# Kernel tuning notes

Measured on AMD Instinct MI355X. Metric: run time of the kernel, lower is better.

The kernel has to match this reference:

```python
import jax, jax.numpy as jnp
import numpy as np

N = 8192   # nodes per graph batch
D = 128    # node_feat_dim
E = 131072 # edges per graph batch
B = 64     # graphs per batch


def _linear_init(k, fin, fout):
    s = 1.0 / np.sqrt(fin)
    kw, kb = jax.random.split(k)
    W = jax.random.uniform(kw, (fin, fout), jnp.float32, -s, s)
    b = jax.random.uniform(kb, (fout,), jnp.float32, -s, s)
    return W, b


def setup_inputs() -> dict:
    key = jax.random.key(0)
    ks = jax.random.split(key, 10)
    x1 = jax.random.normal(ks[0], (N, D), jnp.float32)
    x2 = jax.random.normal(ks[1], (N, D), jnp.float32)
    edge_index1 = jax.random.randint(ks[2], (2, E), 0, N)
    edge_index2 = jax.random.randint(ks[3], (2, E), 0, N)
    # block-contiguous graph ids; every graph id present on both sides
    batch = jnp.arange(N, dtype=jnp.int32) // (N // B)
    mW1, mb1 = _linear_init(ks[4], 2 * D, 512)
    mW2, mb2 = _linear_init(ks[5], 512, 256)  # 256 == 2*D (update_net constraint)
    uW1, ub1 = _linear_init(ks[6], 4 * D, 512)
    uW2, ub2 = _linear_init(ks[7], 512, 256)
    uW3, ub3 = _linear_init(ks[8], 256, D)
    return dict(x1=x1, edge_index1=edge_index1, batch1=batch,
                x2=x2, edge_index2=edge_index2, batch2=batch,
                mW1=mW1, mb1=mb1, mW2=mW2, mb2=mb2,
                uW1=uW1, ub1=ub1, uW2=uW2, ub2=ub2, uW3=uW3, ub3=ub3)


def _message_aggr(x, edge_index, mW1, mb1, mW2, mb2):
    tgt, src = edge_index[0], edge_index[1]
    inp = jnp.concatenate([x[src], x[tgt]], axis=-1)          # [E, 2D]
    msg = jax.nn.relu(inp @ mW1 + mb1) @ mW2 + mb2            # [E, 2D]
    return jax.ops.segment_sum(msg, tgt, num_segments=x.shape[0])


def _cross_attention(x1, batch1, x2, batch2):
    scores = x1 @ x2.T                                        # [N1, N2]
    mask = batch1[:, None] == batch2[None, :]
    scores = jnp.where(mask, scores, -jnp.inf)
    att1 = x1 - jax.nn.softmax(scores, axis=1) @ x2
    att2 = x2 - jax.nn.softmax(scores, axis=0).T @ x1
    return att1, att2


def _node_update(x, messages, attentions, uW1, ub1, uW2, ub2, uW3, ub3):
    u = jnp.concatenate([messages, attentions, x], axis=-1)   # [N, 4D]
    h = jax.nn.relu(u @ uW1 + ub1)
    h = jax.nn.relu(h @ uW2 + ub2)
    return x + h @ uW3 + ub3                                  # residual update


def reference(x1, edge_index1, batch1, x2, edge_index2, batch2,
              mW1, mb1, mW2, mb2, uW1, ub1, uW2, ub2, uW3, ub3):
    m1 = _message_aggr(x1, edge_index1, mW1, mb1, mW2, mb2)
    m2 = _message_aggr(x2, edge_index2, mW1, mb1, mW2, mb2)
    a1, a2 = _cross_attention(x1, batch1, x2, batch2)
    new_x1 = _node_update(x1, m1, a1, uW1, ub1, uW2, ub2, uW3, ub3)
    new_x2 = _node_update(x2, m2, a2, uW1, ub1, uW2, ub2, uW3, ub3)
    return new_x1, new_x2
```

## Files before the change

### kernel.cpp

```cpp
#include <hip/hip_runtime.h>
#include <stdint.h>


typedef unsigned short u16;
typedef __bf16 bf16x8 __attribute__((ext_vector_type(8)));
typedef float f32x4 __attribute__((ext_vector_type(4)));

#define NN 8192
#define DD 128
#define EE 131072
#define GS 128
#define NG 64

__device__ __forceinline__ float bf2f(u16 u){
  return __uint_as_float(((uint32_t)u) << 16);
}
__device__ __forceinline__ u16 f2bf(float f){
  uint32_t x = __float_as_uint(f);
  return (u16)((x + 0x7fffu + ((x >> 16) & 1u)) >> 16);
}
__device__ __forceinline__ void gload16(const u16* g, u16* l){
  __builtin_amdgcn_global_load_lds(
      (const __attribute__((address_space(1))) uint32_t*)(uintptr_t)g,
      (__attribute__((address_space(3))) uint32_t*)(uintptr_t)l, 16, 0, 0);
}
template<int N>
__device__ __forceinline__ void wbar(){
  if constexpr (N == 0)      asm volatile("s_waitcnt vmcnt(0)" ::: "memory");
  else if constexpr (N == 1) asm volatile("s_waitcnt vmcnt(1)" ::: "memory");
  else if constexpr (N == 2) asm volatile("s_waitcnt vmcnt(2)" ::: "memory");
  else if constexpr (N == 4) asm volatile("s_waitcnt vmcnt(4)" ::: "memory");
  else if constexpr (N == 6) asm volatile("s_waitcnt vmcnt(6)" ::: "memory");
  __builtin_amdgcn_s_barrier();
  __builtin_amdgcn_sched_barrier(0);
}
__device__ __forceinline__ void bar(){
  __builtin_amdgcn_s_barrier();
  __builtin_amdgcn_sched_barrier(0);
}

__device__ __forceinline__ void pq_gemm(
    const u16* __restrict__ A, const u16* __restrict__ Wt,
    const float* __restrict__ bias, u16* __restrict__ out,
    int bx, int by, u16* __restrict__ sh, int t)
{
  u16* As = sh;
  u16* Bs = sh + 16384;
  const int brow = by << 7, bcol = bx << 7;
  const int w = t >> 6, lane = t & 63;
  const int rb = (w >> 1) << 6, cb = (w & 1) << 6;
  const int lr = lane & 15, lq = lane >> 4;

  #pragma unroll
  for (int i = 0; i < 8; i++){
    int sg = i * 256 + t;
    int r = sg >> 4, p = sg & 15;
    int l = p ^ (r & 7);
    gload16(A  + (size_t)(brow + r) * 128 + (l << 3), As + sg * 8);
    gload16(Wt + (size_t)(bcol + r) * 128 + (l << 3), Bs + sg * 8);
  }
  wbar<0>();

  f32x4 acc[4][4];
  #pragma unroll
  for (int i = 0; i < 4; i++)
    #pragma unroll
    for (int j = 0; j < 4; j++) acc[i][j] = (f32x4){0.f, 0.f, 0.f, 0.f};

  #pragma unroll
  for (int kb = 0; kb < 4; kb++){
    bf16x8 af[4], bfr[4];
    #pragma unroll
    for (int mi = 0; mi < 4; mi++){
      int row = rb + mi * 16 + lr;
      af[mi] = *(const bf16x8*)&As[(row << 7) + ((((kb << 2) | lq) ^ (row & 7)) << 3)];
    }
    #pragma unroll
    for (int ni = 0; ni < 4; ni++){
      int row = cb + ni * 16 + lr;
      bfr[ni] = *(const bf16x8*)&Bs[(row << 7) + ((((kb << 2) | lq) ^ (row & 7)) << 3)];
    }
    #pragma unroll
    for (int mi = 0; mi < 4; mi++)
      #pragma unroll
      for (int ni = 0; ni < 4; ni++)
        acc[mi][ni] = __builtin_amdgcn_mfma_f32_16x16x32_bf16(af[mi], bfr[ni], acc[mi][ni], 0, 0, 0);
  }

  #pragma unroll
  for (int mi = 0; mi < 4; mi++)
    #pragma unroll
    for (int ni = 0; ni < 4; ni++)
      #pragma unroll
      for (int rr = 0; rr < 4; rr++){
        int grow = brow + rb + mi * 16 + lq * 4 + rr;
        int gcol = bcol + cb + ni * 16 + lr;
        out[(size_t)grow * 1024 + gcol] = f2bf(acc[mi][ni][rr] + bias[gcol]);
      }
}

__global__ __launch_bounds__(256)
void pre_k(const float* __restrict__ mW1, const float* __restrict__ mb1,
           const float* __restrict__ mW2, const float* __restrict__ uW1,
           const float* __restrict__ uW2, const float* __restrict__ uW3,
           const float* __restrict__ x1, const float* __restrict__ x2,
           const int* __restrict__ ei1, const int* __restrict__ ei2,
           u16* __restrict__ WtPQ, float* __restrict__ bPQ,
           u16* __restrict__ Wtm2, u16* __restrict__ Wtu1,
           u16* __restrict__ Wtu2, u16* __restrict__ Wtu3,
           u16* __restrict__ xb, u16* __restrict__ xt,
           u16* __restrict__ U, int* __restrict__ deg)
{
  __shared__ u16 T[8704];
  int b = blockIdx.x, t = threadIdx.x;
  if (b < 168){
    const float* srcs[6] = {mW1, mW1 + 128 * 512, mW2, uW1, uW2, uW3};
    u16* dsts[6] = {WtPQ, WtPQ + 512 * 128, Wtm2, Wtu1, Wtu2, Wtu3};
    const int ldSs[6] = {512, 512, 256, 512, 256, 128};
    const int ldDs[6] = {128, 128, 512, 512, 512, 256};
    const int jb[7]   = {0, 16, 32, 64, 128, 160, 168};
    int j = 0;
    while (b >= jb[j + 1]) j++;
    const int l = b - jb[j];
    const int ldS = ldSs[j], ldD = ldDs[j];
    const int ntc = ldS >> 6;
    const int k0 = (l / ntc) << 6, c0 = (l % ntc) << 6;
    const float* S = srcs[j];
    u16* D = dsts[j];
    #pragma unroll
    for (int i = 0; i < 4; i++){
      int s = i * 256 + t;
      int r = s >> 4, c4 = (s & 15) << 2;
      float4 v = *(const float4*)&S[(size_t)(k0 + r) * ldS + c0 + c4];
      uint2 pk;
      pk.x = (uint32_t)f2bf(v.x) | ((uint32_t)f2bf(v.y) << 16);
      pk.y = (uint32_t)f2bf(v.z) | ((uint32_t)f2bf(v.w) << 16);
      *(uint2*)&T[r * 68 + c4] = pk;
    }
    __syncthreads();
    #pragma unroll
    for (int i = 0; i < 4; i++){
      int s = i * 256 + t;
      int c = s >> 4, k4 = (s & 15) << 2;
      uint32_t a0 = T[(k4 + 0) * 68 + c];
      uint32_t a1 = T[(k4 + 1) * 68 + c];
      uint32_t a2 = T[(k4 + 2) * 68 + c];
      uint32_t a3 = T[(k4 + 3) * 68 + c];
      uint2 pk; pk.x = a0 | (a1 << 16); pk.y = a2 | (a3 << 16);
      *(uint2*)&D[(size_t)(c0 + c) * ldD + k0 + k4] = pk;
    }
  } else if (b == 168){
    #pragma unroll
    for (int i = 0; i < 4; i++){
      int idx = i * 256 + t;
      bPQ[idx] = (idx < 512) ? 0.f : mb1[idx - 512];
    }
  } else if (b < 2217){
    int a = b - 169;
    int side = a >> 10, blk = a & 1023;
    const float* x = side ? x2 : x1;
    int i4 = blk * 256 + t;
    float4 v = *(const float4*)&x[(size_t)i4 * 4];
    uint2 pk;
    pk.x = (uint32_t)f2bf(v.x) | ((uint32_t)f2bf(v.y) << 16);
    pk.y = (uint32_t)f2bf(v.z) | ((uint32_t)f2bf(v.w) << 16);
    *(uint2*)&xb[(size_t)side * NN * DD + (size_t)i4 * 4] = pk;
    int n = i4 >> 5, d = (i4 << 2) & 127;
    *(uint2*)&U[((size_t)side * NN + n) * 512 + 384 + d] = pk;
  } else if (b < 2473){
    int a = b - 2217;
    int side = a >> 7, blk = a & 127;
    const float* x = side ? x2 : x1;
    u16* dst = xt + (size_t)side * DD * NN;
    const int n0 = blk * 64;
    #pragma unroll
    for (int i = 0; i < 8; i++){
      int s = i * 256 + t;
      int r = s >> 5, c4 = (s & 31) << 2;
      float4 v = *(const float4*)&x[(size_t)(n0 + r) * DD + c4];
      uint2 pk;
      pk.x = (uint32_t)f2bf(v.x) | ((uint32_t)f2bf(v.y) << 16);
      pk.y = (uint32_t)f2bf(v.z) | ((uint32_t)f2bf(v.w) << 16);
      *(uint2*)&T[r * 136 + c4] = pk;
    }
    __syncthreads();
    #pragma unroll
    for (int i = 0; i < 8; i++){
      int s = i * 256 + t;
      int d = s >> 4, n4 = (s & 15) << 2;
      uint32_t a0 = T[(n4 + 0) * 136 + d];
      uint32_t a1 = T[(n4 + 1) * 136 + d];
      uint32_t a2 = T[(n4 + 2) * 136 + d];
      uint32_t a3 = T[(n4 + 3) * 136 + d];
      uint2 pk; pk.x = a0 | (a1 << 16); pk.y = a2 | (a3 << 16);
      *(uint2*)(dst + (size_t)d * NN + n0 + n4) = pk;
    }
  } else {
    int a = b - 2473;
    int side = a >> 9, blk = a & 511;
    const int* ei = side ? ei2 : ei1;
    int e = blk * 256 + t;
    atomicAdd(&deg[side * NN + ei[e]], 1);
  }
}

__global__ __launch_bounds__(256)
void scan_k(const int* __restrict__ deg,
            int* __restrict__ offs1, int* __restrict__ cur1,
            int* __restrict__ offs2, int* __restrict__ cur2){
  const int* d = deg + blockIdx.x * NN;
  int* offs = blockIdx.x ? offs2 : offs1;
  int* cur  = blockIdx.x ? cur2  : cur1;
  __shared__ int part[256];
  const int t = threadIdx.x;
  const int base = t * 32;
  int loc[32];
  int s = 0;
  #pragma unroll
  for (int i = 0; i < 32; i++){ loc[i] = s; s += d[base + i]; }
  part[t] = s;
  __syncthreads();
  for (int off = 1; off < 256; off <<= 1){
    int v = (t >= off) ? part[t - off] : 0;
    __syncthreads();
    part[t] += v;
    __syncthreads();
  }
  int pre = (t == 0) ? 0 : part[t - 1];
  #pragma unroll
  for (int i = 0; i < 32; i++){
    int o = pre + loc[i];
    offs[base + i] = o;
    cur[base + i]  = o;
  }
  if (t == 255) offs[NN] = part[255];
}

__global__ __launch_bounds__(256)
void mid_k(const u16* __restrict__ xb, const u16* __restrict__ WtPQ,
           const float* __restrict__ bPQ, u16* __restrict__ PQ,
           const int* __restrict__ ei1, const int* __restrict__ ei2,
           int* __restrict__ cur1, int* __restrict__ cur2,
           int* __restrict__ srt1, int* __restrict__ srt2,
           const u16* __restrict__ xt, u16* __restrict__ U)
{
  __shared__ u16 sh[32768];
  const int b = blockIdx.x, t = threadIdx.x;
  if (b < 1024){
    pq_gemm(xb, WtPQ, bPQ, PQ, b >> 7, b & 127, sh, t);
    return;
  }
  if (b < 2048){
    int a = b - 1024;
    int side = a >> 9, blk = a & 511;
    const int* ei = side ? ei2 : ei1;
    int* cur = side ? cur2 : cur1;
    int* srt = side ? srt2 : srt1;
    int e = blk * 256 + t;
    int tgt = ei[e], src = ei[EE + e];
    int p = atomicAdd(&cur[tgt], 1);
    srt[p] = src;
    return;
  }
  const int a = b - 2048;
  const int side = a >> 7;
  const int g = a & 63, h = (a >> 6) & 1;
  const u16* Xa = xb + (size_t)side * NN * DD;
  const u16* Xb = xb + (size_t)(1 - side) * NN * DD;
  const u16* Xt = xt + (size_t)(1 - side) * DD * NN;
  u16* Uside = U + (size_t)side * NN * 512;

  u16* XaS = sh;
  u16* XbS = sh + 8704;

  const int w = t >> 6, lane = t & 63;
  const int lr = lane & 15, lq = lane >> 4;

  {
    const u16* sa = Xa + ((size_t)g * GS + h * 64) * DD;
    #pragma unroll
    for (int i = 0; i < 4; i++){
      int s = i * 256 + t; int r = s >> 4, c8 = (s & 15) << 3;
      *(uint4*)&XaS[r * 136 + c8] = *(const uint4*)(sa + (size_t)r * DD + c8);
    }
    const u16* sb = Xb + (size_t)g * GS * DD;
    #pragma unroll
    for (int i = 0; i < 8; i++){
      int s = i * 256 + t; int r = s >> 4, c8 = (s & 15) << 3;
      *(uint4*)&XbS[r * 136 + c8] = *(const uint4*)(sb + (size_t)r * DD + c8);
    }
  }
  __syncthreads();

  f32x4 sc[8];
  #pragma unroll
  for (int ct = 0; ct < 8; ct++) sc[ct] = (f32x4){0.f, 0.f, 0.f, 0.f};
  #pragma unroll
  for (int kb = 0; kb < 4; kb++){
    bf16x8 aa = *(const bf16x8*)&XaS[(w * 16 + lr) * 136 + kb * 32 + (lq << 3)];
    #pragma unroll
    for (int ct = 0; ct < 8; ct++){
      bf16x8 bb = *(const bf16x8*)&XbS[(ct * 16 + lr) * 136 + kb * 32 + (lq << 3)];
      sc[ct] = __builtin_amdgcn_mfma_f32_16x16x32_bf16(aa, bb, sc[ct], 0, 0, 0);
    }
  }
  float inv[4];
  #pragma unroll
  for (int rr = 0; rr < 4; rr++){
    float m = sc[0][rr];
    #pragma unroll
    for (int ct = 1; ct < 8; ct++) m = fmaxf(m, sc[ct][rr]);
    #pragma unroll
    for (int sh_ = 1; sh_ < 16; sh_ <<= 1) m = fmaxf(m, __shfl_xor(m, sh_, 64));
    float s = 0.f;
    #pragma unroll
    for (int ct = 0; ct < 8; ct++){
      float e = __expf(sc[ct][rr] - m);
      sc[ct][rr] = e; s += e;
    }
    #pragma unroll
    for (int sh_ = 1; sh_ < 16; sh_ <<= 1) s += __shfl_xor(s, sh_, 64);
    inv[rr] = 1.f / s;
  }
  #pragma unroll
  for (int ct = 0; ct < 8; ct++)
    #pragma unroll
    for (int rr = 0; rr < 4; rr++)
      XaS[(w * 16 + lq * 4 + rr) * 136 + ct * 16 + lr] = f2bf(sc[ct][rr] * inv[rr]);
  __syncthreads();

  f32x4 o[8];
  #pragma unroll
  for (int ct = 0; ct < 8; ct++) o[ct] = (f32x4){0.f, 0.f, 0.f, 0.f};
  #pragma unroll
  for (int kb = 0; kb < 4; kb++){
    bf16x8 aa = *(const bf16x8*)&XaS[(w * 16 + lr) * 136 + kb * 32 + (lq << 3)];
    #pragma unroll
    for (int ct = 0; ct < 8; ct++){
      bf16x8 bb = *(const bf16x8*)(Xt + (size_t)(ct * 16 + lr) * NN + g * GS + kb * 32 + (lq << 3));
      o[ct] = __builtin_amdgcn_mfma_f32_16x16x32_bf16(aa, bb, o[ct], 0, 0, 0);
    }
  }
  const u16* XaG = Xa + ((size_t)g * GS + h * 64) * DD;
  #pragma unroll
  for (int ct = 0; ct < 8; ct++)
    #pragma unroll
    for (int rr = 0; rr < 4; rr++){
      int row = w * 16 + lq * 4 + rr, col = ct * 16 + lr;
      float xa = bf2f(XaG[(size_t)row * DD + col]);
      Uside[((size_t)g * GS + h * 64 + row) * 512 + 256 + col] = f2bf(xa - o[ct][rr]);
    }
}

__global__ __launch_bounds__(256)
void gather_k(const int* __restrict__ offs1, const int* __restrict__ srt1,
              const int* __restrict__ offs2, const int* __restrict__ srt2,
              const u16* __restrict__ PQ, u16* __restrict__ S)
{
  const int side = blockIdx.y;
  const int* offs = side ? offs2 : offs1;
  const int* srt  = side ? srt2  : srt1;
  const u16* base = PQ + (size_t)side * NN * 1024;
  u16* Sb = S + (size_t)side * NN * 512;

  const int node = (blockIdx.x << 2) + (threadIdx.x >> 6);
  const int lane = threadIdx.x & 63;
  const int beg = offs[node], end = offs[node + 1];
  const u16* lbase = base + (lane << 3);

  uint4 qv = *(const uint4*)(base + (size_t)node * 1024 + 512 + (lane << 3));
  float q[8];
  {
    uint32_t qw[4] = {qv.x, qv.y, qv.z, qv.w};
    #pragma unroll
    for (int i = 0; i < 4; i++){
      q[i * 2]     = bf2f((u16)(qw[i] & 0xffffu));
      q[i * 2 + 1] = bf2f((u16)(qw[i] >> 16));
    }
  }
  float acc[8] = {0.f,0.f,0.f,0.f,0.f,0.f,0.f,0.f};

  int e = beg;
  for (; e + 15 < end; e += 16){
    int sx[16];
    #pragma unroll
    for (int i = 0; i < 16; i++) sx[i] = srt[e + i];
    uint4 pv[16];
    #pragma unroll
    for (int i = 0; i < 16; i++)
      pv[i] = *(const uint4*)(lbase + (size_t)sx[i] * 1024);
    #pragma unroll
    for (int i = 0; i < 16; i++){
      uint32_t w0[4] = {pv[i].x, pv[i].y, pv[i].z, pv[i].w};
      #pragma unroll
      for (int j = 0; j < 4; j++){
        acc[j*2]   += fmaxf(bf2f((u16)(w0[j] & 0xffffu)) + q[j*2],   0.f);
        acc[j*2+1] += fmaxf(bf2f((u16)(w0[j] >> 16))     + q[j*2+1], 0.f);
      }
    }
  }
  for (; e + 7 < end; e += 8){
    int sx[8];
    #pragma unroll
    for (int i = 0; i < 8; i++) sx[i] = srt[e + i];
    uint4 pv[8];
    #pragma unroll
    for (int i = 0; i < 8; i++)
      pv[i] = *(const uint4*)(lbase + (size_t)sx[i] * 1024);
    #pragma unroll
    for (int i = 0; i < 8; i++){
      uint32_t w0[4] = {pv[i].x, pv[i].y, pv[i].z, pv[i].w};
      #pragma unroll
      for (int j = 0; j < 4; j++){
        acc[j*2]   += fmaxf(bf2f((u16)(w0[j] & 0xffffu)) + q[j*2],   0.f);
        acc[j*2+1] += fmaxf(bf2f((u16)(w0[j] >> 16))     + q[j*2+1], 0.f);
      }
    }
  }
  for (; e + 3 < end; e += 4){
    int sx[4];
    #pragma unroll
    for (int i = 0; i < 4; i++) sx[i] = srt[e + i];
    uint4 pv[4];
    #pragma unroll
    for (int i = 0; i < 4; i++)
      pv[i] = *(const uint4*)(lbase + (size_t)sx[i] * 1024);
    #pragma unroll
    for (int i = 0; i < 4; i++){
      uint32_t w0[4] = {pv[i].x, pv[i].y, pv[i].z, pv[i].w};
      #pragma unroll
      for (int j = 0; j < 4; j++){
        acc[j*2]   += fmaxf(bf2f((u16)(w0[j] & 0xffffu)) + q[j*2],   0.f);
        acc[j*2+1] += fmaxf(bf2f((u16)(w0[j] >> 16))     + q[j*2+1], 0.f);
      }
    }
  }
  for (; e < end; e++){
    int sA = srt[e];
    uint4 pA = *(const uint4*)(lbase + (size_t)sA * 1024);
    uint32_t aw[4] = {pA.x, pA.y, pA.z, pA.w};
    #pragma unroll
    for (int i = 0; i < 4; i++){
      acc[i*2]   += fmaxf(bf2f((u16)(aw[i] & 0xffffu)) + q[i*2],   0.f);
      acc[i*2+1] += fmaxf(bf2f((u16)(aw[i] >> 16))     + q[i*2+1], 0.f);
    }
  }
  uint4 pk;
  pk.x = (uint32_t)f2bf(acc[0]) | ((uint32_t)f2bf(acc[1]) << 16);
  pk.y = (uint32_t)f2bf(acc[2]) | ((uint32_t)f2bf(acc[3]) << 16);
  pk.z = (uint32_t)f2bf(acc[4]) | ((uint32_t)f2bf(acc[5]) << 16);
  pk.w = (uint32_t)f2bf(acc[6]) | ((uint32_t)f2bf(acc[7]) << 16);
  *(uint4*)(Sb + (size_t)node * 512 + (lane << 3)) = pk;
}

__global__ __launch_bounds__(256, 2)
void upd_k(const u16* __restrict__ Sg,
           const u16* __restrict__ Wtm2, const float* __restrict__ mb2,
           const int* __restrict__ deg, u16* __restrict__ U,
           const u16* __restrict__ Wtu1, const float* __restrict__ ub1,
           const u16* __restrict__ Wtu2, const float* __restrict__ ub2,
           const u16* __restrict__ Wtu3, const float* __restrict__ ub3,
           const float* __restrict__ x1, const float* __restrict__ x2,
           float* __restrict__ out)
{
  __shared__ u16 sh[40960];
  u16* H1s  = sh;
  u16* H2s  = sh + 16384;
  u16* Bst0 = sh + 24576;
  u16* Bst1 = sh + 32768;

  const int t = threadIdx.x;
  const int wc = t >> 6, lane = t & 63;
  const int lr = lane & 15, lq = lane >> 4;
  const int r0 = blockIdx.x << 5;

  const int s0 = t, s1 = t + 256, s2 = t + 512, s3 = t + 768;
  const int c0 = s0 >> 2, c1 = s1 >> 2, c2 = s2 >> 2, c3 = s3 >> 2;
  const int sw0 = (((s0 & 3) ^ (c0 & 3)) << 3);
  const int sw1 = (((s1 & 3) ^ (c1 & 3)) << 3);
  const int sw2 = (((s2 & 3) ^ (c2 & 3)) << 3);
  const int sw3 = (((s3 & 3) ^ (c3 & 3)) << 3);
  const int swr = ((lq ^ (lr & 3)) << 3);

  f32x4 acc[2][4];
  auto zacc = [&](){
    #pragma unroll
    for (int i = 0; i < 2; i++)
      #pragma unroll
      for (int j = 0; j < 4; j++) acc[i][j] = (f32x4){0.f, 0.f, 0.f, 0.f};
  };
  bf16x8 afA[2], afB[2];
  auto compA = [&](const bf16x8 (&af)[2], const u16* Bsb){
    bf16x8 bfv[4];
    #pragma unroll
    for (int ct = 0; ct < 4; ct++)
      bfv[ct] = *(const bf16x8*)&Bsb[(wc * 64 + ct * 16 + lr) * 32 + swr];
    #pragma unroll
    for (int mi = 0; mi < 2; mi++)
      #pragma unroll
      for (int ct = 0; ct < 4; ct++)
        acc[mi][ct] = __builtin_amdgcn_mfma_f32_16x16x32_bf16(af[mi], bfv[ct], acc[mi][ct], 0, 0, 0);
  };

  zacc();
  {
    auto ldS = [&](int kb, bf16x8 (&af)[2]){
      #pragma unroll
      for (int mi = 0; mi < 2; mi++)
        af[mi] = *(const bf16x8*)&Sg[(size_t)(r0 + mi * 16 + lr) * 512 + kb + (lq << 3)];
    };
    auto stB = [&](int kb, u16* dst){
      gload16(Wtm2 + (size_t)c0 * 512 + kb + sw0, dst + s0 * 8);
      gload16(Wtm2 + (size_t)c1 * 512 + kb + sw1, dst + s1 * 8);
      gload16(Wtm2 + (size_t)c2 * 512 + kb + sw2, dst + s2 * 8);
      gload16(Wtm2 + (size_t)c3 * 512 + kb + sw3, dst + s3 * 8);
    };
    stB(0, Bst0);
    ldS(0, afA);
    for (int i2 = 0; i2 < 8; i2++){
      const int kb = i2 << 6;
      stB(kb + 32, Bst1); ldS(kb + 32, afB);
      wbar<6>();
      compA(afA, Bst0);
      bar();
      if (i2 < 7){
        stB(kb + 64, Bst0); ldS(kb + 64, afA);
        wbar<6>();
      } else {
        wbar<0>();
      }
      compA(afB, Bst1);
      bar();
    }
    #pragma unroll
    for (int mi = 0; mi < 2; mi++)
      #pragma unroll
      for (int ct = 0; ct < 4; ct++)
        #pragma unroll
        for (int rr = 0; rr < 4; rr++){
          int row = mi * 16 + lq * 4 + rr;
          int col = wc * 64 + ct * 16 + lr;
          int grow = r0 + row;
          float v = acc[mi][ct][rr] + (float)deg[grow] * mb2[col];
          U[(size_t)grow * 512 + col] = f2bf(v);
        }
  }
  wbar<0>();

  auto ldA = [&](int kb, bf16x8 (&af)[2]){
    #pragma unroll
    for (int mi = 0; mi < 2; mi++)
      af[mi] = *(const bf16x8*)&U[(size_t)(r0 + mi * 16 + lr) * 512 + kb + (lq << 3)];
  };
  for (int hN = 0; hN < 2; hN++){
    zacc();
    auto stB = [&](int kb, u16* dst){
      gload16(Wtu1 + (size_t)(hN * 256 + c0) * 512 + kb + sw0, dst + s0 * 8);
      gload16(Wtu1 + (size_t)(hN * 256 + c1) * 512 + kb + sw1, dst + s1 * 8);
      gload16(Wtu1 + (size_t)(hN * 256 + c2) * 512 + kb + sw2, dst + s2 * 8);
      gload16(Wtu1 + (size_t)(hN * 256 + c3) * 512 + kb + sw3, dst + s3 * 8);
    };
    stB(0, Bst0);
    ldA(0, afA);
    for (int i2 = 0; i2 < 8; i2++){
      const int kb = i2 << 6;
      stB(kb + 32, Bst1); ldA(kb + 32, afB);
      wbar<6>();
      compA(afA, Bst0);
      bar();
      if (i2 < 7){
        stB(kb + 64, Bst0); ldA(kb + 64, afA);
        wbar<6>();
      } else {
        wbar<0>();
      }
      compA(afB, Bst1);
      bar();
    }
    #pragma unroll
    for (int mi = 0; mi < 2; mi++)
      #pragma unroll
      for (int ct = 0; ct < 4; ct++)
        #pragma unroll
        for (int rr = 0; rr < 4; rr++){
          int row = mi * 16 + lq * 4 + rr;
          int gcol = hN * 256 + wc * 64 + ct * 16 + lr;
          float v = acc[mi][ct][rr] + ub1[gcol];
          H1s[(row << 9) + (gcol ^ ((row & 7) << 3))] = f2bf(fmaxf(v, 0.f));
        }
  }
  __syncthreads();

  zacc();
  {
    auto stB = [&](int kb, u16* dst){
      gload16(Wtu2 + (size_t)c0 * 512 + kb + sw0, dst + s0 * 8);
      gload16(Wtu2 + (size_t)c1 * 512 + kb + sw1, dst + s1 * 8);
      gload16(Wtu2 + (size_t)c2 * 512 + kb + sw2, dst + s2 * 8);
      gload16(Wtu2 + (size_t)c3 * 512 + kb + sw3, dst + s3 * 8);
    };
    auto comp = [&](int kb, const u16* Bsb){
      bf16x8 af[2], bfv[4];
      #pragma unroll
      for (int mi = 0; mi < 2; mi++){
        int row = mi * 16 + lr;
        af[mi] = *(const bf16x8*)&H1s[(row << 9) + ((kb + (lq << 3)) ^ ((row & 7) << 3))];
      }
      #pragma unroll
      for (int ct = 0; ct < 4; ct++)
        bfv[ct] = *(const bf16x8*)&Bsb[(wc * 64 + ct * 16 + lr) * 32 + swr];
      #pragma unroll
      for (int mi = 0; mi < 2; mi++)
        #pragma unroll
        for (int ct = 0; ct < 4; ct++)
          acc[mi][ct] = __builtin_amdgcn_mfma_f32_16x16x32_bf16(af[mi], bfv[ct], acc[mi][ct], 0, 0, 0);
    };
    stB(0, Bst0);
    for (int i2 = 0; i2 < 8; i2++){
      const int kb = i2 << 6;
      stB(kb + 32, Bst1);
      wbar<4>();
      comp(kb, Bst0);
      bar();
      if (i2 < 7){
        stB(kb + 64, Bst0);
        wbar<4>();
      } else {
        wbar<0>();
      }
      comp(kb + 32, Bst1);
      bar();
    }
    #pragma unroll
    for (int mi = 0; mi < 2; mi++)
      #pragma unroll
      for (int ct = 0; ct < 4; ct++)
        #pragma unroll
        for (int rr = 0; rr < 4; rr++){
          int row = mi * 16 + lq * 4 + rr;
          int col = wc * 64 + ct * 16 + lr;
          float v = fmaxf(acc[mi][ct][rr] + ub2[col], 0.f);
          H2s[(row << 8) + (col ^ ((row & 7) << 3))] = f2bf(v);
        }
  }
  __syncthreads();

  zacc();
  {
    auto stB = [&](int kb, u16* dst){
      gload16(Wtu3 + (size_t)c0 * 256 + kb + sw0, dst + s0 * 8);
      gload16(Wtu3 + (size_t)c1 * 256 + kb + sw1, dst + s1 * 8);
    };
    auto comp = [&](int kb, const u16* Bsb){
      bf16x8 af[2], bfv[2];
      #pragma unroll
      for (int mi = 0; mi < 2; mi++){
        int row = mi * 16 + lr;
        af[mi] = *(const bf16x8*)&H2s[(row << 8) + ((kb + (lq << 3)) ^ ((row & 7) << 3))];
      }
      #pragma unroll
      for (int ct = 0; ct < 2; ct++)
        bfv[ct] = *(const bf16x8*)&Bsb[(wc * 32 + ct * 16 + lr) * 32 + swr];
      #pragma unroll
      for (int mi = 0; mi < 2; mi++)
        #pragma unroll
        for (int ct = 0; ct < 2; ct++)
          acc[mi][ct] = __builtin_amdgcn_mfma_f32_16x16x32_bf16(af[mi], bfv[ct], acc[mi][ct], 0, 0, 0);
    };
    stB(0, Bst0);
    for (int i2 = 0; i2 < 4; i2++){
      const int kb = i2 << 6;
      stB(kb + 32, Bst1);
      wbar<2>();
      comp(kb, Bst0);
      bar();
      if (i2 < 3){
        stB(kb + 64, Bst0);
        wbar<2>();
      } else {
        wbar<0>();
      }
      comp(kb + 32, Bst1);
      bar();
    }
    #pragma unroll
    for (int mi = 0; mi < 2; mi++)
      #pragma unroll
      for (int ct = 0; ct < 2; ct++)
        #pragma unroll
        for (int rr = 0; rr < 4; rr++){
          int row = mi * 16 + lq * 4 + rr;
          int col = wc * 32 + ct * 16 + lr;
          int grow = r0 + row;
          const float* rp = (grow < NN) ? x1 : x2;
          float v = acc[mi][ct][rr] + ub3[col]
                  + rp[(size_t)(grow & (NN - 1)) * 128 + col];
          out[(size_t)grow * 128 + col] = v;
        }
  }
}

extern "C" void kernel_launch(void* const* d_in, const int* in_sizes, int n_in,
                              void* d_out, int out_size, void* d_ws, size_t ws_size,
                              hipStream_t stream)
{
  const float* x1  = (const float*)d_in[0];
  const int*   ei1 = (const int*)  d_in[1];
  const float* x2  = (const float*)d_in[3];
  const int*   ei2 = (const int*)  d_in[4];
  const float* mW1 = (const float*)d_in[6];
  const float* mb1 = (const float*)d_in[7];
  const float* mW2 = (const float*)d_in[8];
  const float* mb2 = (const float*)d_in[9];
  const float* uW1 = (const float*)d_in[10];
  const float* ub1 = (const float*)d_in[11];
  const float* uW2 = (const float*)d_in[12];
  const float* ub2 = (const float*)d_in[13];
  const float* uW3 = (const float*)d_in[14];
  const float* ub3 = (const float*)d_in[15];
  float* out = (float*)d_out;

  char* w = (char*)d_ws;
  auto alloc = [&](size_t b){ char* p = w; w += (b + 255) & ~(size_t)255; return p; };
  u16*  S    = (u16*)alloc((size_t)2 * NN * 512 * 2);
  u16*  PQ   = (u16*)alloc((size_t)2 * NN * 1024 * 2);
  u16*  xb   = (u16*)alloc((size_t)2 * NN * DD * 2);
  u16*  xt   = (u16*)alloc((size_t)2 * DD * NN * 2);
  u16*  U    = (u16*)alloc((size_t)2 * NN * 512 * 2);
  int*  deg  = (int*)alloc((size_t)2 * NN * 4);
  int*  offs1 = (int*)alloc((NN + 1) * 4);
  int*  offs2 = (int*)alloc((NN + 1) * 4);
  int*  cur1  = (int*)alloc(NN * 4);
  int*  cur2  = (int*)alloc(NN * 4);
  int*  srt1  = (int*)alloc((size_t)EE * 4);
  int*  srt2  = (int*)alloc((size_t)EE * 4);
  u16*  WtPQ = (u16*)alloc(1024 * 128 * 2);
  float* bPQ = (float*)alloc(1024 * 4);
  u16*  Wtm2 = (u16*)alloc(256 * 512 * 2);
  u16*  Wtu1 = (u16*)alloc(512 * 512 * 2);
  u16*  Wtu2 = (u16*)alloc(256 * 512 * 2);
  u16*  Wtu3 = (u16*)alloc(128 * 256 * 2);

  hipMemsetAsync(deg, 0, (size_t)2 * NN * 4, stream);

  pre_k<<<3497, 256, 0, stream>>>(
      mW1, mb1, mW2, uW1, uW2, uW3, x1, x2, ei1, ei2,
      WtPQ, bPQ, Wtm2, Wtu1, Wtu2, Wtu3, xb, xt, U, deg);

  scan_k<<<2, 256, 0, stream>>>(deg, offs1, cur1, offs2, cur2);

  mid_k<<<2304, 256, 0, stream>>>(xb, WtPQ, bPQ, PQ, ei1, ei2,
                                  cur1, cur2, srt1, srt2, xt, U);

  gather_k<<<dim3(NN / 4, 2), 256, 0, stream>>>(offs1, srt1, offs2, srt2, PQ, S);

  upd_k<<<512, 256, 0, stream>>>(S, Wtm2, mb2, deg, U,
                                 Wtu1, ub1, Wtu2, ub2, Wtu3, ub3,
                                 x1, x2, out);
}
```

Before: 223.4 us.

## Load update-MLP weight fragments directly from global instead of LDS staging

In the fused update kernel, the double-buffered global-to-LDS weight staging (global_load_lds with swizzle and barriers) is removed. Each wave now reads its weight fragments straight from global memory into registers inside simple unrolled K loops. This cuts the LDS footprint from 80KB to 48KB and removes many block barriers, which should raise occupancy and reduce sync overhead. In exchange, weight loads lose explicit prefetch and rely on the cache and compiler scheduling to hide latency. The launch-bounds minimum-occupancy hint is also dropped, and the wbar/bar helpers are simplified, which could affect other kernels that used them.

```diff
diff --git a/kernel.cpp b/kernel.cpp
--- a/kernel.cpp
+++ b/kernel.cpp
@@ -27,14 +27,6 @@
 template<int N>
 __device__ __forceinline__ void wbar(){
   if constexpr (N == 0)      asm volatile("s_waitcnt vmcnt(0)" ::: "memory");
-  else if constexpr (N == 1) asm volatile("s_waitcnt vmcnt(1)" ::: "memory");
-  else if constexpr (N == 2) asm volatile("s_waitcnt vmcnt(2)" ::: "memory");
-  else if constexpr (N == 4) asm volatile("s_waitcnt vmcnt(4)" ::: "memory");
-  else if constexpr (N == 6) asm volatile("s_waitcnt vmcnt(6)" ::: "memory");
-  __builtin_amdgcn_s_barrier();
-  __builtin_amdgcn_sched_barrier(0);
-}
-__device__ __forceinline__ void bar(){
   __builtin_amdgcn_s_barrier();
   __builtin_amdgcn_sched_barrier(0);
 }
@@ -453,7 +445,7 @@
   *(uint4*)(Sb + (size_t)node * 512 + (lane << 3)) = pk;
 }
 
-__global__ __launch_bounds__(256, 2)
+__global__ __launch_bounds__(256)
 void upd_k(const u16* __restrict__ Sg,
            const u16* __restrict__ Wtm2, const float* __restrict__ mb2,
            const int* __restrict__ deg, u16* __restrict__ U,
@@ -463,25 +455,15 @@
            const float* __restrict__ x1, const float* __restrict__ x2,
            float* __restrict__ out)
 {
-  __shared__ u16 sh[40960];
-  u16* H1s  = sh;
-  u16* H2s  = sh + 16384;
-  u16* Bst0 = sh + 24576;
-  u16* Bst1 = sh + 32768;
+  __shared__ u16 sh[24576];
+  u16* H1s = sh;
+  u16* H2s = sh + 16384;
 
   const int t = threadIdx.x;
   const int wc = t >> 6, lane = t & 63;
   const int lr = lane & 15, lq = lane >> 4;
   const int r0 = blockIdx.x << 5;
 
-  const int s0 = t, s1 = t + 256, s2 = t + 512, s3 = t + 768;
-  const int c0 = s0 >> 2, c1 = s1 >> 2, c2 = s2 >> 2, c3 = s3 >> 2;
-  const int sw0 = (((s0 & 3) ^ (c0 & 3)) << 3);
-  const int sw1 = (((s1 & 3) ^ (c1 & 3)) << 3);
-  const int sw2 = (((s2 & 3) ^ (c2 & 3)) << 3);
-  const int sw3 = (((s3 & 3) ^ (c3 & 3)) << 3);
-  const int swr = ((lq ^ (lr & 3)) << 3);
-
   f32x4 acc[2][4];
   auto zacc = [&](){
     #pragma unroll
@@ -489,93 +471,53 @@
       #pragma unroll
       for (int j = 0; j < 4; j++) acc[i][j] = (f32x4){0.f, 0.f, 0.f, 0.f};
   };
-  bf16x8 afA[2], afB[2];
-  auto compA = [&](const bf16x8 (&af)[2], const u16* Bsb){
-    bf16x8 bfv[4];
+
+  zacc();
+  #pragma unroll 4
+  for (int kb = 0; kb < 512; kb += 32){
+    bf16x8 af[2], bfv[4];
+    #pragma unroll
+    for (int mi = 0; mi < 2; mi++)
+      af[mi] = *(const bf16x8*)&Sg[(size_t)(r0 + mi * 16 + lr) * 512 + kb + (lq << 3)];
     #pragma unroll
     for (int ct = 0; ct < 4; ct++)
-      bfv[ct] = *(const bf16x8*)&Bsb[(wc * 64 + ct * 16 + lr) * 32 + swr];
+      bfv[ct] = *(const bf16x8*)&Wtm2[(size_t)(wc * 64 + ct * 16 + lr) * 512 + kb + (lq << 3)];
     #pragma unroll
     for (int mi = 0; mi < 2; mi++)
       #pragma unroll
       for (int ct = 0; ct < 4; ct++)
         acc[mi][ct] = __builtin_amdgcn_mfma_f32_16x16x32_bf16(af[mi], bfv[ct], acc[mi][ct], 0, 0, 0);
-  };
-
-  zacc();
-  {
-    auto ldS = [&](int kb, bf16x8 (&af)[2]){
-      #pragma unroll
-      for (int mi = 0; mi < 2; mi++)
-        af[mi] = *(const bf16x8*)&Sg[(size_t)(r0 + mi * 16 + lr) * 512 + kb + (lq << 3)];
-    };
-    auto stB = [&](int kb, u16* dst){
-      gload16(Wtm2 + (size_t)c0 * 512 + kb + sw0, dst + s0 * 8);
-      gload16(Wtm2 + (size_t)c1 * 512 + kb + sw1, dst + s1 * 8);
-      gload16(Wtm2 + (size_t)c2 * 512 + kb + sw2, dst + s2 * 8);
-      gload16(Wtm2 + (size_t)c3 * 512 + kb + sw3, dst + s3 * 8);
-    };
-    stB(0, Bst0);
-    ldS(0, afA);
-    for (int i2 = 0; i2 < 8; i2++){
-      const int kb = i2 << 6;
-      stB(kb + 32, Bst1); ldS(kb + 32, afB);
-      wbar<6>();
-      compA(afA, Bst0);
-      bar();
-      if (i2 < 7){
-        stB(kb + 64, Bst0); ldS(kb + 64, afA);
-        wbar<6>();
-      } else {
-        wbar<0>();
+  }
+  #pragma unroll
+  for (int mi = 0; mi < 2; mi++)
+    #pragma unroll
+    for (int ct = 0; ct < 4; ct++)
+      #pragma unroll
+      for (int rr = 0; rr < 4; rr++){
+        int row = mi * 16 + lq * 4 + rr;
+        int col = wc * 64 + ct * 16 + lr;
+        int grow = r0 + row;
+        float v = acc[mi][ct][rr] + (float)deg[grow] * mb2[col];
+        U[(size_t)grow * 512 + col] = f2bf(v);
       }
-      compA(afB, Bst1);
-      bar();
-    }
-    #pragma unroll
-    for (int mi = 0; mi < 2; mi++)
-      #pragma unroll
-      for (int ct = 0; ct < 4; ct++)
-        #pragma unroll
-        for (int rr = 0; rr < 4; rr++){
-          int row = mi * 16 + lq * 4 + rr;
-          int col = wc * 64 + ct * 16 + lr;
-          int grow = r0 + row;
-          float v = acc[mi][ct][rr] + (float)deg[grow] * mb2[col];
-          U[(size_t)grow * 512 + col] = f2bf(v);
-        }
-  }
   wbar<0>();
 
-  auto ldA = [&](int kb, bf16x8 (&af)[2]){
-    #pragma unroll
-    for (int mi = 0; mi < 2; mi++)
-      af[mi] = *(const bf16x8*)&U[(size_t)(r0 + mi * 16 + lr) * 512 + kb + (lq << 3)];
-  };
   for (int hN = 0; hN < 2; hN++){
     zacc();
-    auto stB = [&](int kb, u16* dst){
-      gload16(Wtu1 + (size_t)(hN * 256 + c0) * 512 + kb + sw0, dst + s0 * 8);
-      gload16(Wtu1 + (size_t)(hN * 256 + c1) * 512 + kb + sw1, dst + s1 * 8);
-      gload16(Wtu1 + (size_t)(hN * 256 + c2) * 512 + kb + sw2, dst + s2 * 8);
-      gload16(Wtu1 + (size_t)(hN * 256 + c3) * 512 + kb + sw3, dst + s3 * 8);
-    };
-    stB(0, Bst0);
-    ldA(0, afA);
-    for (int i2 = 0; i2 < 8; i2++){
-      const int kb = i2 << 6;
-      stB(kb + 32, Bst1); ldA(kb + 32, afB);
-      wbar<6>();
-      compA(afA, Bst0);
-      bar();
-      if (i2 < 7){
-        stB(kb + 64, Bst0); ldA(kb + 64, afA);
-        wbar<6>();
-      } else {
-        wbar<0>();
-      }
-      compA(afB, Bst1);
-      bar();
+    #pragma unroll 4
+    for (int kb = 0; kb < 512; kb += 32){
+      bf16x8 af[2], bfv[4];
+      #pragma unroll
+      for (int mi = 0; mi < 2; mi++)
+        af[mi] = *(const bf16x8*)&U[(size_t)(r0 + mi * 16 + lr) * 512 + kb + (lq << 3)];
+      #pragma unroll
+      for (int ct = 0; ct < 4; ct++)
+        bfv[ct] = *(const bf16x8*)&Wtu1[(size_t)(hN * 256 + wc * 64 + ct * 16 + lr) * 512 + kb + (lq << 3)];
+      #pragma unroll
+      for (int mi = 0; mi < 2; mi++)
+        #pragma unroll
+        for (int ct = 0; ct < 4; ct++)
+          acc[mi][ct] = __builtin_amdgcn_mfma_f32_16x16x32_bf16(af[mi], bfv[ct], acc[mi][ct], 0, 0, 0);
     }
     #pragma unroll
     for (int mi = 0; mi < 2; mi++)
@@ -592,112 +534,68 @@
   __syncthreads();
 
   zacc();
-  {
-    auto stB = [&](int kb, u16* dst){
-      gload16(Wtu2 + (size_t)c0 * 512 + kb + sw0, dst + s0 * 8);
-      gload16(Wtu2 + (size_t)c1 * 512 + kb + sw1, dst + s1 * 8);
-      gload16(Wtu2 + (size_t)c2 * 512 + kb + sw2, dst + s2 * 8);
-      gload16(Wtu2 + (size_t)c3 * 512 + kb + sw3, dst + s3 * 8);
-    };
-    auto comp = [&](int kb, const u16* Bsb){
-      bf16x8 af[2], bfv[4];
-      #pragma unroll
-      for (int mi = 0; mi < 2; mi++){
-        int row = mi * 16 + lr;
-        af[mi] = *(const bf16x8*)&H1s[(row << 9) + ((kb + (lq << 3)) ^ ((row & 7) << 3))];
+  #pragma unroll 4
+  for (int kb = 0; kb < 512; kb += 32){
+    bf16x8 af[2], bfv[4];
+    #pragma unroll
+    for (int mi = 0; mi < 2; mi++){
+      int row = mi * 16 + lr;
+      af[mi] = *(const bf16x8*)&H1s[(row << 9) + ((kb + (lq << 3)) ^ ((row & 7) << 3))];
+    }
+    #pragma unroll
+    for (int ct = 0; ct < 4; ct++)
+      bfv[ct] = *(const bf16x8*)&Wtu2[(size_t)(wc * 64 + ct * 16 + lr) * 512 + kb + (lq << 3)];
+    #pragma unroll
+    for (int mi = 0; mi < 2; mi++)
+      #pragma unroll
+      for (int ct = 0; ct < 4; ct++)
+        acc[mi][ct] = __builtin_amdgcn_mfma_f32_16x16x32_bf16(af[mi], bfv[ct], acc[mi][ct], 0, 0, 0);
+  }
+  #pragma unroll
+  for (int mi = 0; mi < 2; mi++)
+    #pragma unroll
+    for (int ct = 0; ct < 4; ct++)
+      #pragma unroll
+      for (int rr = 0; rr < 4; rr++){
+        int row = mi * 16 + lq * 4 + rr;
+        int col = wc * 64 + ct * 16 + lr;
+        float v = fmaxf(acc[mi][ct][rr] + ub2[col], 0.f);
+        H2s[(row << 8) + (col ^ ((row & 7) << 3))] = f2bf(v);
       }
-      #pragma unroll
-      for (int ct = 0; ct < 4; ct++)
-        bfv[ct] = *(const bf16x8*)&Bsb[(wc * 64 + ct * 16 + lr) * 32 + swr];
-      #pragma unroll
-      for (int mi = 0; mi < 2; mi++)
-        #pragma unroll
-        for (int ct = 0; ct < 4; ct++)
-          acc[mi][ct] = __builtin_amdgcn_mfma_f32_16x16x32_bf16(af[mi], bfv[ct], acc[mi][ct], 0, 0, 0);
-    };
-    stB(0, Bst0);
-    for (int i2 = 0; i2 < 8; i2++){
-      const int kb = i2 << 6;
-      stB(kb + 32, Bst1);
-      wbar<4>();
-      comp(kb, Bst0);
-      bar();
-      if (i2 < 7){
-        stB(kb + 64, Bst0);
-        wbar<4>();
-      } else {
-        wbar<0>();
+  __syncthreads();
+
+  zacc();
+  #pragma unroll 4
+  for (int kb = 0; kb < 256; kb += 32){
+    bf16x8 af[2], bfv[2];
+    #pragma unroll
+    for (int mi = 0; mi < 2; mi++){
+      int row = mi * 16 + lr;
+      af[mi] = *(const bf16x8*)&H2s[(row << 8) + ((kb + (lq << 3)) ^ ((row & 7) << 3))];
+    }
+    #pragma unroll
+    for (int ct = 0; ct < 2; ct++)
+      bfv[ct] = *(const bf16x8*)&Wtu3[(size_t)(wc * 32 + ct * 16 + lr) * 256 + kb + (lq << 3)];
+    #pragma unroll
+    for (int mi = 0; mi < 2; mi++)
+      #pragma unroll
+      for (int ct = 0; ct < 2; ct++)
+        acc[mi][ct] = __builtin_amdgcn_mfma_f32_16x16x32_bf16(af[mi], bfv[ct], acc[mi][ct], 0, 0, 0);
+  }
+  #pragma unroll
+  for (int mi = 0; mi < 2; mi++)
+    #pragma unroll
+    for (int ct = 0; ct < 2; ct++)
+      #pragma unroll
+      for (int rr = 0; rr < 4; rr++){
+        int row = mi * 16 + lq * 4 + rr;
+        int col = wc * 32 + ct * 16 + lr;
+        int grow = r0 + row;
+        const float* rp = (grow < NN) ? x1 : x2;
+        float v = acc[mi][ct][rr] + ub3[col]
+                + rp[(size_t)(grow & (NN - 1)) * 128 + col];
+        out[(size_t)grow * 128 + col] = v;
       }
-      comp(kb + 32, Bst1);
-      bar();
-    }
-    #pragma unroll
-    for (int mi = 0; mi < 2; mi++)
-      #pragma unroll
-      for (int ct = 0; ct < 4; ct++)
-        #pragma unroll
-        for (int rr = 0; rr < 4; rr++){
-          int row = mi * 16 + lq * 4 + rr;
-          int col = wc * 64 + ct * 16 + lr;
-          float v = fmaxf(acc[mi][ct][rr] + ub2[col], 0.f);
-          H2s[(row << 8) + (col ^ ((row & 7) << 3))] = f2bf(v);
-        }
-  }
-  __syncthreads();
-
-  zacc();
-  {
-    auto stB = [&](int kb, u16* dst){
-      gload16(Wtu3 + (size_t)c0 * 256 + kb + sw0, dst + s0 * 8);
-      gload16(Wtu3 + (size_t)c1 * 256 + kb + sw1, dst + s1 * 8);
-    };
-    auto comp = [&](int kb, const u16* Bsb){
-      bf16x8 af[2], bfv[2];
-      #pragma unroll
-      for (int mi = 0; mi < 2; mi++){
-        int row = mi * 16 + lr;
-        af[mi] = *(const bf16x8*)&H2s[(row << 8) + ((kb + (lq << 3)) ^ ((row & 7) << 3))];
-      }
-      #pragma unroll
-      for (int ct = 0; ct < 2; ct++)
-        bfv[ct] = *(const bf16x8*)&Bsb[(wc * 32 + ct * 16 + lr) * 32 + swr];
-      #pragma unroll
-      for (int mi = 0; mi < 2; mi++)
-        #pragma unroll
-        for (int ct = 0; ct < 2; ct++)
-          acc[mi][ct] = __builtin_amdgcn_mfma_f32_16x16x32_bf16(af[mi], bfv[ct], acc[mi][ct], 0, 0, 0);
-    };
-    stB(0, Bst0);
-    for (int i2 = 0; i2 < 4; i2++){
-      const int kb = i2 << 6;
-      stB(kb + 32, Bst1);
-      wbar<2>();
-      comp(kb, Bst0);
-      bar();
-      if (i2 < 3){
-        stB(kb + 64, Bst0);
-        wbar<2>();
-      } else {
-        wbar<0>();
-      }
-      comp(kb + 32, Bst1);
-      bar();
-    }
-    #pragma unroll
-    for (int mi = 0; mi < 2; mi++)
-      #pragma unroll
-      for (int ct = 0; ct < 2; ct++)
-        #pragma unroll
-        for (int rr = 0; rr < 4; rr++){
-          int row = mi * 16 + lq * 4 + rr;
-          int col = wc * 32 + ct * 16 + lr;
-          int grow = r0 + row;
-          const float* rp = (grow < NN) ? x1 : x2;
-          float v = acc[mi][ct][rr] + ub3[col]
-                  + rp[(size_t)(grow & (NN - 1)) * 128 + col];
-          out[(size_t)grow * 128 + col] = v;
-        }
-  }
 }
 
 extern "C" void kernel_launch(void* const* d_in, const int* in_sizes, int n_in,
```

Measured after the change: 262.1 us. 17.3% more time.
